# Optimization experiments

Hardware: AMD Instinct MI355X
Metric: run time of the kernel (lower is better)

## Reference

```python
import jax, jax.numpy as jnp
import numpy as np
from jax import lax


def setup_inputs() -> dict:
    key = jax.random.key(0)
    ks = jax.random.split(key, 8)
    B, S, H, L = 64, 512, 768, 9
    hidden = jax.random.normal(ks[0], (B, S, H), jnp.float32)
    label = jax.random.randint(ks[1], (B, S), 0, L, dtype=jnp.int32)
    mask = jnp.ones((B, S), jnp.int32)
    W = jax.random.normal(ks[2], (H, L), jnp.float32) * 0.02
    b = jnp.zeros((L,), jnp.float32)
    start_transitions = jax.random.normal(ks[3], (L,), jnp.float32) * 0.1
    end_transitions = jax.random.normal(ks[4], (L,), jnp.float32) * 0.1
    transitions = jax.random.normal(ks[5], (L, L), jnp.float32) * 0.1
    return dict(hidden=hidden, label=label, mask=mask, W=W, b=b,
                start_transitions=start_transitions,
                end_transitions=end_transitions,
                transitions=transitions)


def reference(hidden, label, mask, W, b, start_transitions, end_transitions, transitions):
    B, S, H = hidden.shape
    L = b.shape[0]
    # output_layer: [B,S,H] @ [H,L] -> emissions, then transpose to time-major [S,B,L]
    emissions = jnp.einsum('bsh,hl->bsl', hidden, W) + b
    em = jnp.transpose(emissions, (1, 0, 2))        # [S, B, L]
    tags = label.T                                   # [S, B]
    m = mask.T.astype(jnp.float32)                   # [S, B]

    def gather_tag(em_t, tag_t):
        # em_t [B,L], tag_t [B] -> [B]
        return jnp.take_along_axis(em_t, tag_t[:, None], axis=1)[:, 0]

    # ---- numerator: score of the gold path ----
    score0 = start_transitions[tags[0]] + gather_tag(em[0], tags[0])
    def num_step(carry, x):
        score, prev = carry
        em_t, tag_t, m_t = x
        s = transitions[prev, tag_t] + gather_tag(em_t, tag_t)
        score = score + s * m_t
        prev = jnp.where(m_t > 0, tag_t, prev)
        return (score, prev), None
    (score, last_gold), _ = lax.scan(num_step, (score0, tags[0]), (em[1:], tags[1:], m[1:]))
    score = score + end_transitions[last_gold]

    # ---- denominator: forward algorithm (logsumexp DP) ----
    alpha0 = start_transitions[None, :] + em[0]      # [B, L]
    def fwd_step(alpha, x):
        em_t, m_t = x
        nxt = jax.nn.logsumexp(alpha[:, :, None] + transitions[None, :, :] + em_t[:, None, :], axis=1)
        alpha = jnp.where(m_t[:, None] > 0, nxt, alpha)
        return alpha, None
    alphaT, _ = lax.scan(fwd_step, alpha0, (em[1:], m[1:]))
    logZ = jax.nn.logsumexp(alphaT + end_transitions[None, :], axis=1)

    llh = jnp.sum(score - logZ)                      # reduction='sum'
    loss = -llh / B

    # ---- Viterbi decode (decode() is called without mask -> full length) ----
    v0 = start_transitions[None, :] + em[0]
    def vit_step(v, em_t):
        scores = v[:, :, None] + transitions[None, :, :] + em_t[:, None, :]  # [B, L, L]
        return jnp.max(scores, axis=1), jnp.argmax(scores, axis=1)
    vT, hist = lax.scan(vit_step, v0, em[1:])        # hist [S-1, B, L]
    last_tag = jnp.argmax(vT + end_transitions[None, :], axis=1)  # [B]
    def back_step(tag, bp_t):
        prev = jnp.take_along_axis(bp_t, tag[:, None], axis=1)[:, 0]
        return prev, prev
    _, prevs = lax.scan(back_step, last_tag, hist, reverse=True)  # [S-1, B]
    path = jnp.concatenate([prevs, last_tag[None, :]], axis=0).T  # [B, S]

    # ---- accuracy bookkeeping (label > 0 mask) ----
    label_flat = label.reshape(-1)
    label_mask = (label_flat > 0).astype(jnp.int32)
    predict = path.reshape(-1).astype(jnp.int32) * label_mask
    correct = jnp.sum((predict == label_flat).astype(jnp.float32))
    return loss, correct, predict, label_flat
```

## Files before the change

kernel.cpp:

```cpp
#include <hip/hip_runtime.h>
#include <hip/hip_bf16.h>

#define NB 64
#define NS 512
#define NH 768
#define NL 9
#define NROWS (NB*NS)
#define EMN (NROWS*NL)

#define VST  4617
#define BPST 4616

__device__ __forceinline__ float readlane_f(float v, int l) {
    return __int_as_float(__builtin_amdgcn_readlane(__float_as_int(v), l));
}
__device__ __forceinline__ unsigned long long readlane_u64(unsigned long long v, int l) {
    unsigned int lo = (unsigned int)__builtin_amdgcn_readlane((int)(unsigned int)(v & 0xffffffffULL), l);
    unsigned int hi = (unsigned int)__builtin_amdgcn_readlane((int)(unsigned int)(v >> 32), l);
    return ((unsigned long long)hi << 32) | (unsigned long long)lo;
}
template <int CTRL>
__device__ __forceinline__ float dpp_add(float x) {
    int t = __builtin_amdgcn_update_dpp(0, __float_as_int(x), CTRL, 0xf, 0xf, false);
    return x + __int_as_float(t);
}
__device__ __forceinline__ float wave_sum_to63(float x) {
    x = dpp_add<0x111>(x);
    x = dpp_add<0x112>(x);
    x = dpp_add<0x114>(x);
    x = dpp_add<0x118>(x);
    x = dpp_add<0x142>(x);
    x = dpp_add<0x143>(x);
    return x;
}
template <int I>
__device__ __forceinline__ float rowbc(float x) {
    return __int_as_float(__builtin_amdgcn_ds_swizzle(__float_as_int(x), (I << 5) | 0x10));
}

__global__ __launch_bounds__(256) void k_gemm(const float* __restrict__ hidden,
                                              const float* __restrict__ W,
                                              const float* __restrict__ bias,
                                              float* __restrict__ em,
                                              float* __restrict__ out) {
    __shared__ float s_part[4][4][NL];
    int tid = threadIdx.x;
    int lane = tid & 63;
    int w = tid >> 6;
    int bx = blockIdx.x;
    if (bx == 0 && tid == 0) { out[0] = 0.f; out[1] = 0.f; }

    int kbase = 192 * w + lane;
    float Wv[3][NL];
#pragma unroll
    for (int c = 0; c < 3; c++) {
        const float* wp = W + (size_t)(kbase + 64 * c) * NL;
#pragma unroll
        for (int j = 0; j < NL; j++) Wv[c][j] = wp[j];
    }

#pragma unroll
    for (int r = 0; r < 4; r++) {
        int row = 4 * bx + r;
        const float* hp = hidden + (size_t)row * NH + kbase;
        float h0 = hp[0], h1 = hp[64], h2 = hp[128];
        float acc[NL];
#pragma unroll
        for (int j = 0; j < NL; j++) {
            acc[j] = fmaf(h0, Wv[0][j], fmaf(h1, Wv[1][j], h2 * Wv[2][j]));
        }
#pragma unroll
        for (int j = 0; j < NL; j++) acc[j] = wave_sum_to63(acc[j]);
        if (lane == 63) {
#pragma unroll
            for (int j = 0; j < NL; j++) s_part[w][r][j] = acc[j];
        }
    }
    __syncthreads();
    if (tid < 36) {
        int r = tid / NL, j = tid % NL;
        float v = (s_part[0][r][j] + s_part[1][r][j]) +
                  (s_part[2][r][j] + s_part[3][r][j]) + bias[j];
        em[(size_t)(4 * bx + r) * NL + j] = v;
    }
}

__global__ __launch_bounds__(256) void k_dp(const float* __restrict__ em,
                                            const int* __restrict__ label,
                                            const int* __restrict__ mask,
                                            const float* __restrict__ startT,
                                            const float* __restrict__ endT,
                                            const float* __restrict__ trans,
                                            float* __restrict__ out) {
    __shared__ float s_T[NL * NL];
    __shared__ int s_mki[4][NS];
    __shared__ float s_v[4 * VST];
    __shared__ unsigned char s_bp[4 * BPST];
    __shared__ unsigned char s_path[4 * NS];

    int bx = blockIdx.x;
    int tid = threadIdx.x;
    int lane = tid & 63;
    bool isfwd = bx < 16;
    int b0 = (isfwd ? bx : (bx - 16)) * 4;

    if (tid < NL * NL) s_T[tid] = trans[tid];
    if (isfwd) {
        for (int q = tid; q < 4 * NS / 4; q += 256)
            ((int4*)s_mki)[q] = ((const int4*)(mask + b0 * NS))[q];
    }
    __syncthreads();

    if (isfwd) {
        if (tid < 64) {
            int bb = lane >> 4;
            int jcol = lane & 15;
            int jcol9 = jcol < NL ? jcol : NL - 1;
            const float* gp = em + (size_t)(b0 + bb) * (NS * NL) + jcol9;
            float Mc0 = __expf(s_T[0 * NL + jcol9]);
            float Mc1 = __expf(s_T[1 * NL + jcol9]);
            float Mc2 = __expf(s_T[2 * NL + jcol9]);
            float Mc3 = __expf(s_T[3 * NL + jcol9]);
            float Mc4 = __expf(s_T[4 * NL + jcol9]);
            float Mc5 = __expf(s_T[5 * NL + jcol9]);
            float Mc6 = __expf(s_T[6 * NL + jcol9]);
            float Mc7 = __expf(s_T[7 * NL + jcol9]);
            float Mc8 = __expf(s_T[8 * NL + jcol9]);
            float a = __expf(startT[jcol9] + gp[0]);
            int eacc = 0;

#define FBODY(EC_, KC_) do { \
    float _w0=rowbc<0>(a),_w1=rowbc<1>(a),_w2=rowbc<2>(a),_w3=rowbc<3>(a),_w4=rowbc<4>(a), \
          _w5=rowbc<5>(a),_w6=rowbc<6>(a),_w7=rowbc<7>(a),_w8=rowbc<8>(a); \
    float _p0=_w0*Mc0,_p1=_w1*Mc1,_p2=_w2*Mc2,_p3=_w3*Mc3,_p4=_w4*Mc4, \
          _p5=_w5*Mc5,_p6=_w6*Mc6,_p7=_w7*Mc7,_p8=_w8*Mc8; \
    float _s=(((_p0+_p1)+(_p2+_p3))+((_p4+_p5)+(_p6+_p7)))+_p8; \
    float _an=(EC_)*_s; \
    a = ((KC_) > 0) ? _an : a; \
} while (0)

#define FREN() do { \
    float _c0=rowbc<0>(a),_c1=rowbc<1>(a),_c2=rowbc<2>(a),_c3=rowbc<3>(a),_c4=rowbc<4>(a), \
          _c5=rowbc<5>(a),_c6=rowbc<6>(a),_c7=rowbc<7>(a),_c8=rowbc<8>(a); \
    float _cc=(((_c0+_c1)+(_c2+_c3))+((_c4+_c5)+(_c6+_c7)))+_c8; \
    int _ex=((__float_as_int(_cc)>>23)&255)-127; \
    a=ldexpf(a,-_ex); eacc+=_ex; \
} while (0)

            float e8[8]; int k8[8];
#pragma unroll
            for (int p = 0; p < 8; p++) {
                e8[p] = __expf(gp[(1 + p) * NL]);
                k8[p] = s_mki[bb][1 + p];
            }
            for (int t0 = 1; t0 <= NS - 15; t0 += 8) {
#pragma unroll
                for (int p = 0; p < 8; p++) {
                    int t = t0 + p;
                    float ec = e8[p]; int kc = k8[p];
                    int tn = t + 8; tn = tn > NS - 1 ? NS - 1 : tn;
                    e8[p] = __expf(gp[tn * NL]);
                    k8[p] = s_mki[bb][tn];
                    FBODY(ec, kc);
                    if (p == 7) FREN();
                }
            }
#pragma unroll
            for (int p = 0; p < 7; p++) FBODY(e8[p], k8[p]);
#undef FBODY
#undef FREN
            float z = a * __expf(endT[jcol9]);
            float c0 = rowbc<0>(z), c1 = rowbc<1>(z), c2 = rowbc<2>(z);
            float c3 = rowbc<3>(z), c4 = rowbc<4>(z), c5 = rowbc<5>(z);
            float c6 = rowbc<6>(z), c7 = rowbc<7>(z), c8 = rowbc<8>(z);
            float c = (((c0 + c1) + (c2 + c3)) + ((c4 + c5) + (c6 + c7))) + c8;
            if (jcol == 0) {
                float lz = (float)eacc * 0.6931471805599453f + __logf(c);
                atomicAdd(out, lz * (1.0f / (float)NB));
            }
        } else if (tid < 128) {
            int g = lane >> 4;
            int ll = lane & 15;
            int b = b0 + g;
            const int* lb = label + b * NS;
            const float* ge = em + (size_t)b * NS * NL;
            int h = 0, sl = 0;
            for (int cch = 0; cch < 4; cch++) {
                int la8[8]; int mk8[8];
#pragma unroll
                for (int r = 0; r < 8; r++) {
                    int t = ll * 32 + cch * 8 + r;
                    la8[r] = lb[t];
                    int m = s_mki[g][t];
                    if (t == 0) m = 1;
                    mk8[r] = m;
                }
#pragma unroll
                for (int r = 0; r < 8; r++) if (mk8[r] > 0) { h = 1; sl = la8[r]; }
            }
#pragma unroll
            for (int d = 1; d < 16; d <<= 1) {
                int ho = __shfl_up(h, d, 16);
                int so = __shfl_up(sl, d, 16);
                if (!h) { h = ho; sl = so; }
            }
            int lg = __shfl(sl, 15, 16);
            int incoming = __shfl_up(sl, 1, 16);
            int labz = lb[0];
            int prevr = (ll == 0) ? labz : incoming;
            float sc = 0.f;
            for (int cch = 0; cch < 4; cch++) {
                int la8[8]; int mk8[8]; float ev8[8];
#pragma unroll
                for (int r = 0; r < 8; r++) {
                    int t = ll * 32 + cch * 8 + r;
                    la8[r] = lb[t];
                    int m = s_mki[g][t];
                    if (t == 0) m = 1;
                    mk8[r] = m;
                }
#pragma unroll
                for (int r = 0; r < 8; r++) {
                    int t = ll * 32 + cch * 8 + r;
                    ev8[r] = ge[t * NL + la8[r]];
                }
#pragma unroll
                for (int r = 0; r < 8; r++) {
                    int t = ll * 32 + cch * 8 + r;
                    if (t > 0) {
                        float s = s_T[prevr * NL + la8[r]] + ev8[r];
                        sc += s * (float)mk8[r];
                    }
                    if (mk8[r] > 0) prevr = la8[r];
                }
            }
            if (ll == 0) sc += startT[labz] + ge[labz] + endT[lg];
#pragma unroll
            for (int d = 1; d < 16; d <<= 1) sc += __shfl_xor(sc, d, 16);
            if (ll == 0) atomicAdd(out, -sc * (1.0f / (float)NB));
        }
    } else {
        if (tid < 64) {
            int bb = lane >> 4;
            int jcol = lane & 15;
            int jcol9 = jcol < NL ? jcol : NL - 1;
            const float* gv = em + (size_t)(b0 + bb) * (NS * NL) + jcol9;
            float Tc0 = s_T[0 * NL + jcol9];
            float Tc1 = s_T[1 * NL + jcol9];
            float Tc2 = s_T[2 * NL + jcol9];
            float Tc3 = s_T[3 * NL + jcol9];
            float Tc4 = s_T[4 * NL + jcol9];
            float Tc5 = s_T[5 * NL + jcol9];
            float Tc6 = s_T[6 * NL + jcol9];
            float Tc7 = s_T[7 * NL + jcol9];
            float Tc8 = s_T[8 * NL + jcol9];
            float v = startT[jcol9] + gv[0];
            int svbase = bb * VST + jcol;
            s_v[svbase] = v;

#define VBODY(EC_, T_) do { \
    float _w0=rowbc<0>(v),_w1=rowbc<1>(v),_w2=rowbc<2>(v),_w3=rowbc<3>(v),_w4=rowbc<4>(v), \
          _w5=rowbc<5>(v),_w6=rowbc<6>(v),_w7=rowbc<7>(v),_w8=rowbc<8>(v); \
    float _m0=_w0+Tc0,_m1=_w1+Tc1,_m2=_w2+Tc2,_m3=_w3+Tc3,_m4=_w4+Tc4, \
          _m5=_w5+Tc5,_m6=_w6+Tc6,_m7=_w7+Tc7,_m8=_w8+Tc8; \
    float _Ma=fmaxf(fmaxf(_m0,_m1),_m2); \
    float _Mb=fmaxf(fmaxf(_m3,_m4),_m5); \
    float _Mc=fmaxf(fmaxf(_m6,_m7),_m8); \
    v = fmaxf(fmaxf(_Ma,_Mb),_Mc) + (EC_); \
    s_v[svbase + (T_) * NL] = v; \
} while (0)

            float e8[8];
#pragma unroll
            for (int p = 0; p < 8; p++) e8[p] = gv[(1 + p) * NL];
            for (int t0 = 1; t0 <= NS - 15; t0 += 8) {
#pragma unroll
                for (int p = 0; p < 8; p++) {
                    int t = t0 + p;
                    float ec = e8[p];
                    int tn = t + 8; tn = tn > NS - 1 ? NS - 1 : tn;
                    e8[p] = gv[tn * NL];
                    VBODY(ec, t);
                }
            }
#pragma unroll
            for (int p = 0; p < 7; p++) VBODY(e8[p], 505 + p);
#undef VBODY
        }
        __syncthreads();
        for (int it = 0; it < 8; it++) {
            int item = tid + it * 256;
            int bb = item >> 9;
            int t = item & (NS - 1);
            if (t > 0) {
                const float* vpp = s_v + bb * VST + (t - 1) * NL;
                const float* ge = em + (size_t)(b0 + bb) * (NS * NL) + t * NL;
                float vp[NL], emt[NL];
#pragma unroll
                for (int i = 0; i < NL; i++) vp[i] = vpp[i];
#pragma unroll
                for (int j = 0; j < NL; j++) emt[j] = ge[j];
#pragma unroll
                for (int j = 0; j < NL; j++) {
                    float e = emt[j];
                    float val[NL];
#pragma unroll
                    for (int i = 0; i < NL; i++) val[i] = (vp[i] + s_T[i * NL + j]) + e;
                    bool c01 = val[0] >= val[1]; float m01 = c01 ? val[0] : val[1]; int i01 = c01 ? 0 : 1;
                    bool c23 = val[2] >= val[3]; float m23 = c23 ? val[2] : val[3]; int i23 = c23 ? 2 : 3;
                    bool c45 = val[4] >= val[5]; float m45 = c45 ? val[4] : val[5]; int i45 = c45 ? 4 : 5;
                    bool c67 = val[6] >= val[7]; float m67 = c67 ? val[6] : val[7]; int i67 = c67 ? 6 : 7;
                    bool ca = m01 >= m23; float ma = ca ? m01 : m23; int ia = ca ? i01 : i23;
                    bool cb = m45 >= m67; float mb = cb ? m45 : m67; int ib = cb ? i45 : i67;
                    bool cc = ma >= mb;  float mc = cc ? ma : mb;  int ic = cc ? ia : ib;
                    bool cd = mc >= val[8]; int bi = cd ? ic : 8;
                    s_bp[bb * BPST + t * NL + j] = (unsigned char)bi;
                }
            }
        }
        __syncthreads();
        {
            int w = tid >> 6;
            const float* sv = s_v + w * VST;
            const unsigned char* bpp = s_bp + w * BPST;
            unsigned char* pth = s_path + w * NS;
            float bb2 = sv[(NS - 1) * NL + 0] + endT[0]; int lt = 0;
#pragma unroll
            for (int jj = 1; jj < NL; jj++) {
                float fj = sv[(NS - 1) * NL + jj] + endT[jj];
                if (fj > bb2) { bb2 = fj; lt = jj; }
            }
            unsigned long long G[8];
#pragma unroll
            for (int r = 0; r < 8; r++) {
                int t0 = (lane * 8 + r) * NL;
                unsigned long long g = 0;
                if (lane == 0 && r == 0) {
                    g = 0x876543210ULL;
                } else {
#pragma unroll
                    for (int x = 0; x < NL; x++) g |= (unsigned long long)bpp[t0 + x] << (4 * x);
                }
                G[r] = g;
            }
            unsigned long long A = 0x876543210ULL;
#pragma unroll
            for (int r = 7; r >= 0; r--) {
                unsigned long long An = 0;
#pragma unroll
                for (int x = 0; x < NL; x++) {
                    int ax = (int)((A >> (4 * x)) & 15ULL);
                    int gvv = (int)((G[r] >> (4 * ax)) & 15ULL);
                    An |= (unsigned long long)gvv << (4 * x);
                }
                A = An;
            }
            int e = 0; int cur = lt;
            for (int llv = 63; llv >= 0; --llv) {
                if (lane == llv) e = cur;
                unsigned long long Al = readlane_u64(A, llv);
                cur = (int)((Al >> (4 * cur)) & 15ULL);
            }
            unsigned long long pw = 0; int c2 = e;
#pragma unroll
            for (int r = 7; r >= 0; r--) {
                pw |= (unsigned long long)c2 << (8 * r);
                c2 = (int)((G[r] >> (4 * c2)) & 15ULL);
            }
            *(unsigned long long*)(pth + lane * 8) = pw;
        }
        __syncthreads();
        float cnt = 0.f;
#pragma unroll
        for (int q = 0; q < 8; q++) {
            int item = tid + q * 256;
            int bb = item >> 9;
            int t = item & (NS - 1);
            int b = b0 + bb;
            int idx = b * NS + t;
            int lab = label[idx];
            int p = (int)s_path[bb * NS + t];
            int pred = (lab > 0) ? p : 0;
            out[2 + idx] = (float)pred;
            out[2 + NROWS + idx] = (float)lab;
            cnt += (pred == lab) ? 1.f : 0.f;
        }
#pragma unroll
        for (int d = 1; d < 64; d <<= 1) cnt += __shfl_xor(cnt, d);
        if ((tid & 63) == 0) atomicAdd(out + 1, cnt);
    }
}

extern "C" void kernel_launch(void* const* d_in, const int* in_sizes, int n_in,
                              void* d_out, int out_size, void* d_ws, size_t ws_size,
                              hipStream_t stream) {
    const float* hidden = (const float*)d_in[0];
    const int*   label  = (const int*)d_in[1];
    const int*   mask   = (const int*)d_in[2];
    const float* W      = (const float*)d_in[3];
    const float* bias   = (const float*)d_in[4];
    const float* startT = (const float*)d_in[5];
    const float* endT   = (const float*)d_in[6];
    const float* trans  = (const float*)d_in[7];
    float* out = (float*)d_out;

    float* em = (float*)d_ws;

    k_gemm<<<8192, 256, 0, stream>>>(hidden, W, bias, em, out);
    k_dp<<<32, 256, 0, stream>>>(em, label, mask, startT, endT, trans, out);
}
```

Measured before the change: 210.9 us.

## Interleave forward-algorithm and Viterbi recurrences in one wavefront per batch group

```diff
diff --git a/kernel.cpp b/kernel.cpp
--- a/kernel.cpp
+++ b/kernel.cpp
@@ -101,294 +101,259 @@
     int bx = blockIdx.x;
     int tid = threadIdx.x;
     int lane = tid & 63;
-    bool isfwd = bx < 16;
-    int b0 = (isfwd ? bx : (bx - 16)) * 4;
+    int b0 = bx * 4;
 
     if (tid < NL * NL) s_T[tid] = trans[tid];
-    if (isfwd) {
-        for (int q = tid; q < 4 * NS / 4; q += 256)
-            ((int4*)s_mki)[q] = ((const int4*)(mask + b0 * NS))[q];
-    }
-    __syncthreads();
-
-    if (isfwd) {
-        if (tid < 64) {
-            int bb = lane >> 4;
-            int jcol = lane & 15;
-            int jcol9 = jcol < NL ? jcol : NL - 1;
-            const float* gp = em + (size_t)(b0 + bb) * (NS * NL) + jcol9;
-            float Mc0 = __expf(s_T[0 * NL + jcol9]);
-            float Mc1 = __expf(s_T[1 * NL + jcol9]);
-            float Mc2 = __expf(s_T[2 * NL + jcol9]);
-            float Mc3 = __expf(s_T[3 * NL + jcol9]);
-            float Mc4 = __expf(s_T[4 * NL + jcol9]);
-            float Mc5 = __expf(s_T[5 * NL + jcol9]);
-            float Mc6 = __expf(s_T[6 * NL + jcol9]);
-            float Mc7 = __expf(s_T[7 * NL + jcol9]);
-            float Mc8 = __expf(s_T[8 * NL + jcol9]);
-            float a = __expf(startT[jcol9] + gp[0]);
-            int eacc = 0;
-
-#define FBODY(EC_, KC_) do { \
-    float _w0=rowbc<0>(a),_w1=rowbc<1>(a),_w2=rowbc<2>(a),_w3=rowbc<3>(a),_w4=rowbc<4>(a), \
-          _w5=rowbc<5>(a),_w6=rowbc<6>(a),_w7=rowbc<7>(a),_w8=rowbc<8>(a); \
-    float _p0=_w0*Mc0,_p1=_w1*Mc1,_p2=_w2*Mc2,_p3=_w3*Mc3,_p4=_w4*Mc4, \
-          _p5=_w5*Mc5,_p6=_w6*Mc6,_p7=_w7*Mc7,_p8=_w8*Mc8; \
-    float _s=(((_p0+_p1)+(_p2+_p3))+((_p4+_p5)+(_p6+_p7)))+_p8; \
-    float _an=(EC_)*_s; \
-    a = ((KC_) > 0) ? _an : a; \
-} while (0)
-
-#define FREN() do { \
-    float _c0=rowbc<0>(a),_c1=rowbc<1>(a),_c2=rowbc<2>(a),_c3=rowbc<3>(a),_c4=rowbc<4>(a), \
-          _c5=rowbc<5>(a),_c6=rowbc<6>(a),_c7=rowbc<7>(a),_c8=rowbc<8>(a); \
-    float _cc=(((_c0+_c1)+(_c2+_c3))+((_c4+_c5)+(_c6+_c7)))+_c8; \
-    int _ex=((__float_as_int(_cc)>>23)&255)-127; \
-    a=ldexpf(a,-_ex); eacc+=_ex; \
-} while (0)
-
-            float e8[8]; int k8[8];
-#pragma unroll
-            for (int p = 0; p < 8; p++) {
-                e8[p] = __expf(gp[(1 + p) * NL]);
-                k8[p] = s_mki[bb][1 + p];
-            }
-            for (int t0 = 1; t0 <= NS - 15; t0 += 8) {
-#pragma unroll
-                for (int p = 0; p < 8; p++) {
-                    int t = t0 + p;
-                    float ec = e8[p]; int kc = k8[p];
-                    int tn = t + 8; tn = tn > NS - 1 ? NS - 1 : tn;
-                    e8[p] = __expf(gp[tn * NL]);
-                    k8[p] = s_mki[bb][tn];
-                    FBODY(ec, kc);
-                    if (p == 7) FREN();
-                }
-            }
-#pragma unroll
-            for (int p = 0; p < 7; p++) FBODY(e8[p], k8[p]);
-#undef FBODY
-#undef FREN
-            float z = a * __expf(endT[jcol9]);
-            float c0 = rowbc<0>(z), c1 = rowbc<1>(z), c2 = rowbc<2>(z);
-            float c3 = rowbc<3>(z), c4 = rowbc<4>(z), c5 = rowbc<5>(z);
-            float c6 = rowbc<6>(z), c7 = rowbc<7>(z), c8 = rowbc<8>(z);
-            float c = (((c0 + c1) + (c2 + c3)) + ((c4 + c5) + (c6 + c7))) + c8;
-            if (jcol == 0) {
-                float lz = (float)eacc * 0.6931471805599453f + __logf(c);
-                atomicAdd(out, lz * (1.0f / (float)NB));
-            }
-        } else if (tid < 128) {
-            int g = lane >> 4;
-            int ll = lane & 15;
-            int b = b0 + g;
-            const int* lb = label + b * NS;
-            const float* ge = em + (size_t)b * NS * NL;
-            int h = 0, sl = 0;
-            for (int cch = 0; cch < 4; cch++) {
-                int la8[8]; int mk8[8];
-#pragma unroll
-                for (int r = 0; r < 8; r++) {
-                    int t = ll * 32 + cch * 8 + r;
-                    la8[r] = lb[t];
-                    int m = s_mki[g][t];
-                    if (t == 0) m = 1;
-                    mk8[r] = m;
-                }
-#pragma unroll
-                for (int r = 0; r < 8; r++) if (mk8[r] > 0) { h = 1; sl = la8[r]; }
-            }
-#pragma unroll
-            for (int d = 1; d < 16; d <<= 1) {
-                int ho = __shfl_up(h, d, 16);
-                int so = __shfl_up(sl, d, 16);
-                if (!h) { h = ho; sl = so; }
-            }
-            int lg = __shfl(sl, 15, 16);
-            int incoming = __shfl_up(sl, 1, 16);
-            int labz = lb[0];
-            int prevr = (ll == 0) ? labz : incoming;
-            float sc = 0.f;
-            for (int cch = 0; cch < 4; cch++) {
-                int la8[8]; int mk8[8]; float ev8[8];
-#pragma unroll
-                for (int r = 0; r < 8; r++) {
-                    int t = ll * 32 + cch * 8 + r;
-                    la8[r] = lb[t];
-                    int m = s_mki[g][t];
-                    if (t == 0) m = 1;
-                    mk8[r] = m;
-                }
-#pragma unroll
-                for (int r = 0; r < 8; r++) {
-                    int t = ll * 32 + cch * 8 + r;
-                    ev8[r] = ge[t * NL + la8[r]];
-                }
-#pragma unroll
-                for (int r = 0; r < 8; r++) {
-                    int t = ll * 32 + cch * 8 + r;
-                    if (t > 0) {
-                        float s = s_T[prevr * NL + la8[r]] + ev8[r];
-                        sc += s * (float)mk8[r];
-                    }
-                    if (mk8[r] > 0) prevr = la8[r];
-                }
-            }
-            if (ll == 0) sc += startT[labz] + ge[labz] + endT[lg];
-#pragma unroll
-            for (int d = 1; d < 16; d <<= 1) sc += __shfl_xor(sc, d, 16);
-            if (ll == 0) atomicAdd(out, -sc * (1.0f / (float)NB));
-        }
-    } else {
-        if (tid < 64) {
-            int bb = lane >> 4;
-            int jcol = lane & 15;
-            int jcol9 = jcol < NL ? jcol : NL - 1;
-            const float* gv = em + (size_t)(b0 + bb) * (NS * NL) + jcol9;
-            float Tc0 = s_T[0 * NL + jcol9];
-            float Tc1 = s_T[1 * NL + jcol9];
-            float Tc2 = s_T[2 * NL + jcol9];
-            float Tc3 = s_T[3 * NL + jcol9];
-            float Tc4 = s_T[4 * NL + jcol9];
-            float Tc5 = s_T[5 * NL + jcol9];
-            float Tc6 = s_T[6 * NL + jcol9];
-            float Tc7 = s_T[7 * NL + jcol9];
-            float Tc8 = s_T[8 * NL + jcol9];
-            float v = startT[jcol9] + gv[0];
-            int svbase = bb * VST + jcol;
-            s_v[svbase] = v;
-
-#define VBODY(EC_, T_) do { \
-    float _w0=rowbc<0>(v),_w1=rowbc<1>(v),_w2=rowbc<2>(v),_w3=rowbc<3>(v),_w4=rowbc<4>(v), \
-          _w5=rowbc<5>(v),_w6=rowbc<6>(v),_w7=rowbc<7>(v),_w8=rowbc<8>(v); \
+    for (int q = tid; q < 4 * NS / 4; q += 256)
+        ((int4*)s_mki)[q] = ((const int4*)(mask + b0 * NS))[q];
+    __syncthreads();
+
+    if (tid < 64) {
+        int bb = lane >> 4;
+        int jcol = lane & 15;
+        int jcol9 = jcol < NL ? jcol : NL - 1;
+        const float* gp = em + (size_t)(b0 + bb) * (NS * NL) + jcol9;
+        float Mc0 = __expf(s_T[0 * NL + jcol9]), Tc0 = s_T[0 * NL + jcol9];
+        float Mc1 = __expf(s_T[1 * NL + jcol9]), Tc1 = s_T[1 * NL + jcol9];
+        float Mc2 = __expf(s_T[2 * NL + jcol9]), Tc2 = s_T[2 * NL + jcol9];
+        float Mc3 = __expf(s_T[3 * NL + jcol9]), Tc3 = s_T[3 * NL + jcol9];
+        float Mc4 = __expf(s_T[4 * NL + jcol9]), Tc4 = s_T[4 * NL + jcol9];
+        float Mc5 = __expf(s_T[5 * NL + jcol9]), Tc5 = s_T[5 * NL + jcol9];
+        float Mc6 = __expf(s_T[6 * NL + jcol9]), Tc6 = s_T[6 * NL + jcol9];
+        float Mc7 = __expf(s_T[7 * NL + jcol9]), Tc7 = s_T[7 * NL + jcol9];
+        float Mc8 = __expf(s_T[8 * NL + jcol9]), Tc8 = s_T[8 * NL + jcol9];
+        float st0 = startT[jcol9] + gp[0];
+        float a = __expf(st0);
+        float v = st0;
+        int eacc = 0;
+        int svbase = bb * VST + jcol;
+        s_v[svbase] = v;
+
+#define SWZ9(SRC_, A0,A1,A2,A3,A4,A5,A6,A7,A8) \
+    float A0 = rowbc<0>(SRC_), A1 = rowbc<1>(SRC_), A2 = rowbc<2>(SRC_); \
+    float A3 = rowbc<3>(SRC_), A4 = rowbc<4>(SRC_), A5 = rowbc<5>(SRC_); \
+    float A6 = rowbc<6>(SRC_), A7 = rowbc<7>(SRC_), A8 = rowbc<8>(SRC_)
+
+#define STEP(EV_, EF_, KC_, T_) do { \
+    SWZ9(v, _w0,_w1,_w2,_w3,_w4,_w5,_w6,_w7,_w8); \
+    SWZ9(a, _q0,_q1,_q2,_q3,_q4,_q5,_q6,_q7,_q8); \
     float _m0=_w0+Tc0,_m1=_w1+Tc1,_m2=_w2+Tc2,_m3=_w3+Tc3,_m4=_w4+Tc4, \
           _m5=_w5+Tc5,_m6=_w6+Tc6,_m7=_w7+Tc7,_m8=_w8+Tc8; \
     float _Ma=fmaxf(fmaxf(_m0,_m1),_m2); \
     float _Mb=fmaxf(fmaxf(_m3,_m4),_m5); \
     float _Mc=fmaxf(fmaxf(_m6,_m7),_m8); \
-    v = fmaxf(fmaxf(_Ma,_Mb),_Mc) + (EC_); \
+    v = fmaxf(fmaxf(_Ma,_Mb),_Mc) + (EV_); \
     s_v[svbase + (T_) * NL] = v; \
+    float _p0=_q0*Mc0,_p1=_q1*Mc1,_p2=_q2*Mc2,_p3=_q3*Mc3,_p4=_q4*Mc4, \
+          _p5=_q5*Mc5,_p6=_q6*Mc6,_p7=_q7*Mc7,_p8=_q8*Mc8; \
+    float _s=(((_p0+_p1)+(_p2+_p3))+((_p4+_p5)+(_p6+_p7)))+_p8; \
+    float _an=(EF_)*_s; \
+    a = ((KC_) > 0) ? _an : a; \
 } while (0)
 
-            float e8[8];
-#pragma unroll
-            for (int p = 0; p < 8; p++) e8[p] = gv[(1 + p) * NL];
-            for (int t0 = 1; t0 <= NS - 15; t0 += 8) {
-#pragma unroll
-                for (int p = 0; p < 8; p++) {
-                    int t = t0 + p;
-                    float ec = e8[p];
-                    int tn = t + 8; tn = tn > NS - 1 ? NS - 1 : tn;
-                    e8[p] = gv[tn * NL];
-                    VBODY(ec, t);
+#define FREN() do { \
+    SWZ9(a, _c0,_c1,_c2,_c3,_c4,_c5,_c6,_c7,_c8); \
+    float _cc=(((_c0+_c1)+(_c2+_c3))+((_c4+_c5)+(_c6+_c7)))+_c8; \
+    int _ex=((__float_as_int(_cc)>>23)&255)-127; \
+    a=ldexpf(a,-_ex); eacc+=_ex; \
+} while (0)
+
+        float ef8[8]; float ev8[8]; int k8[8];
+#pragma unroll
+        for (int p = 0; p < 8; p++) {
+            float raw = gp[(1 + p) * NL];
+            ev8[p] = raw;
+            ef8[p] = __expf(raw);
+            k8[p] = s_mki[bb][1 + p];
+        }
+        for (int t0 = 1; t0 <= NS - 15; t0 += 8) {
+#pragma unroll
+            for (int p = 0; p < 8; p++) {
+                int t = t0 + p;
+                float ecv = ev8[p]; float ecf = ef8[p]; int kc = k8[p];
+                int tn = t + 8; tn = tn > NS - 1 ? NS - 1 : tn;
+                float raw = gp[tn * NL];
+                ev8[p] = raw;
+                ef8[p] = __expf(raw);
+                k8[p] = s_mki[bb][tn];
+                STEP(ecv, ecf, kc, t);
+                if (p == 7) FREN();
+            }
+        }
+#pragma unroll
+        for (int p = 0; p < 7; p++) STEP(ev8[p], ef8[p], k8[p], 505 + p);
+#undef STEP
+#undef FREN
+        float z = a * __expf(endT[jcol9]);
+        SWZ9(z, zc0,zc1,zc2,zc3,zc4,zc5,zc6,zc7,zc8);
+        float c = (((zc0 + zc1) + (zc2 + zc3)) + ((zc4 + zc5) + (zc6 + zc7))) + zc8;
+        if (jcol == 0) {
+            float lz = (float)eacc * 0.6931471805599453f + __logf(c);
+            atomicAdd(out, lz * (1.0f / (float)NB));
+        }
+#undef SWZ9
+    } else if (tid < 128) {
+        int g = lane >> 4;
+        int ll = lane & 15;
+        int b = b0 + g;
+        const int* lb = label + b * NS;
+        const float* ge = em + (size_t)b * NS * NL;
+        int h = 0, sl = 0;
+        for (int cch = 0; cch < 4; cch++) {
+            int la8[8]; int mk8[8];
+#pragma unroll
+            for (int r = 0; r < 8; r++) {
+                int t = ll * 32 + cch * 8 + r;
+                la8[r] = lb[t];
+                int m = s_mki[g][t];
+                if (t == 0) m = 1;
+                mk8[r] = m;
+            }
+#pragma unroll
+            for (int r = 0; r < 8; r++) if (mk8[r] > 0) { h = 1; sl = la8[r]; }
+        }
+#pragma unroll
+        for (int d = 1; d < 16; d <<= 1) {
+            int ho = __shfl_up(h, d, 16);
+            int so = __shfl_up(sl, d, 16);
+            if (!h) { h = ho; sl = so; }
+        }
+        int lg = __shfl(sl, 15, 16);
+        int incoming = __shfl_up(sl, 1, 16);
+        int labz = lb[0];
+        int prevr = (ll == 0) ? labz : incoming;
+        float sc = 0.f;
+        for (int cch = 0; cch < 4; cch++) {
+            int la8[8]; int mk8[8]; float ev8[8];
+#pragma unroll
+            for (int r = 0; r < 8; r++) {
+                int t = ll * 32 + cch * 8 + r;
+                la8[r] = lb[t];
+                int m = s_mki[g][t];
+                if (t == 0) m = 1;
+                mk8[r] = m;
+            }
+#pragma unroll
+            for (int r = 0; r < 8; r++) {
+                int t = ll * 32 + cch * 8 + r;
+                ev8[r] = ge[t * NL + la8[r]];
+            }
+#pragma unroll
+            for (int r = 0; r < 8; r++) {
+                int t = ll * 32 + cch * 8 + r;
+                if (t > 0) {
+                    float s = s_T[prevr * NL + la8[r]] + ev8[r];
+                    sc += s * (float)mk8[r];
                 }
-            }
-#pragma unroll
-            for (int p = 0; p < 7; p++) VBODY(e8[p], 505 + p);
-#undef VBODY
-        }
-        __syncthreads();
-        for (int it = 0; it < 8; it++) {
-            int item = tid + it * 256;
-            int bb = item >> 9;
-            int t = item & (NS - 1);
-            if (t > 0) {
-                const float* vpp = s_v + bb * VST + (t - 1) * NL;
-                const float* ge = em + (size_t)(b0 + bb) * (NS * NL) + t * NL;
-                float vp[NL], emt[NL];
-#pragma unroll
-                for (int i = 0; i < NL; i++) vp[i] = vpp[i];
-#pragma unroll
-                for (int j = 0; j < NL; j++) emt[j] = ge[j];
-#pragma unroll
-                for (int j = 0; j < NL; j++) {
-                    float e = emt[j];
-                    float val[NL];
-#pragma unroll
-                    for (int i = 0; i < NL; i++) val[i] = (vp[i] + s_T[i * NL + j]) + e;
-                    bool c01 = val[0] >= val[1]; float m01 = c01 ? val[0] : val[1]; int i01 = c01 ? 0 : 1;
-                    bool c23 = val[2] >= val[3]; float m23 = c23 ? val[2] : val[3]; int i23 = c23 ? 2 : 3;
-                    bool c45 = val[4] >= val[5]; float m45 = c45 ? val[4] : val[5]; int i45 = c45 ? 4 : 5;
-                    bool c67 = val[6] >= val[7]; float m67 = c67 ? val[6] : val[7]; int i67 = c67 ? 6 : 7;
-                    bool ca = m01 >= m23; float ma = ca ? m01 : m23; int ia = ca ? i01 : i23;
-                    bool cb = m45 >= m67; float mb = cb ? m45 : m67; int ib = cb ? i45 : i67;
-                    bool cc = ma >= mb;  float mc = cc ? ma : mb;  int ic = cc ? ia : ib;
-                    bool cd = mc >= val[8]; int bi = cd ? ic : 8;
-                    s_bp[bb * BPST + t * NL + j] = (unsigned char)bi;
-                }
-            }
-        }
-        __syncthreads();
-        {
-            int w = tid >> 6;
-            const float* sv = s_v + w * VST;
-            const unsigned char* bpp = s_bp + w * BPST;
-            unsigned char* pth = s_path + w * NS;
-            float bb2 = sv[(NS - 1) * NL + 0] + endT[0]; int lt = 0;
-#pragma unroll
-            for (int jj = 1; jj < NL; jj++) {
-                float fj = sv[(NS - 1) * NL + jj] + endT[jj];
-                if (fj > bb2) { bb2 = fj; lt = jj; }
-            }
-            unsigned long long G[8];
-#pragma unroll
-            for (int r = 0; r < 8; r++) {
-                int t0 = (lane * 8 + r) * NL;
-                unsigned long long g = 0;
-                if (lane == 0 && r == 0) {
-                    g = 0x876543210ULL;
-                } else {
-#pragma unroll
-                    for (int x = 0; x < NL; x++) g |= (unsigned long long)bpp[t0 + x] << (4 * x);
-                }
-                G[r] = g;
-            }
-            unsigned long long A = 0x876543210ULL;
-#pragma unroll
-            for (int r = 7; r >= 0; r--) {
-                unsigned long long An = 0;
-#pragma unroll
-                for (int x = 0; x < NL; x++) {
-                    int ax = (int)((A >> (4 * x)) & 15ULL);
-                    int gvv = (int)((G[r] >> (4 * ax)) & 15ULL);
-                    An |= (unsigned long long)gvv << (4 * x);
-                }
-                A = An;
-            }
-            int e = 0; int cur = lt;
-            for (int llv = 63; llv >= 0; --llv) {
-                if (lane == llv) e = cur;
-                unsigned long long Al = readlane_u64(A, llv);
-                cur = (int)((Al >> (4 * cur)) & 15ULL);
-            }
-            unsigned long long pw = 0; int c2 = e;
-#pragma unroll
-            for (int r = 7; r >= 0; r--) {
-                pw |= (unsigned long long)c2 << (8 * r);
-                c2 = (int)((G[r] >> (4 * c2)) & 15ULL);
-            }
-            *(unsigned long long*)(pth + lane * 8) = pw;
-        }
-        __syncthreads();
-        float cnt = 0.f;
-#pragma unroll
-        for (int q = 0; q < 8; q++) {
-            int item = tid + q * 256;
-            int bb = item >> 9;
-            int t = item & (NS - 1);
-            int b = b0 + bb;
-            int idx = b * NS + t;
-            int lab = label[idx];
-            int p = (int)s_path[bb * NS + t];
-            int pred = (lab > 0) ? p : 0;
-            out[2 + idx] = (float)pred;
-            out[2 + NROWS + idx] = (float)lab;
-            cnt += (pred == lab) ? 1.f : 0.f;
-        }
-#pragma unroll
-        for (int d = 1; d < 64; d <<= 1) cnt += __shfl_xor(cnt, d);
-        if ((tid & 63) == 0) atomicAdd(out + 1, cnt);
-    }
+                if (mk8[r] > 0) prevr = la8[r];
+            }
+        }
+        if (ll == 0) sc += startT[labz] + ge[labz] + endT[lg];
+#pragma unroll
+        for (int d = 1; d < 16; d <<= 1) sc += __shfl_xor(sc, d, 16);
+        if (ll == 0) atomicAdd(out, -sc * (1.0f / (float)NB));
+    }
+    __syncthreads();
+    for (int it = 0; it < 8; it++) {
+        int item = tid + it * 256;
+        int bb = item >> 9;
+        int t = item & (NS - 1);
+        if (t > 0) {
+            const float* vpp = s_v + bb * VST + (t - 1) * NL;
+            const float* ge = em + (size_t)(b0 + bb) * (NS * NL) + t * NL;
+            float vp[NL], emt[NL];
+#pragma unroll
+            for (int i = 0; i < NL; i++) vp[i] = vpp[i];
+#pragma unroll
+            for (int j = 0; j < NL; j++) emt[j] = ge[j];
+#pragma unroll
+            for (int j = 0; j < NL; j++) {
+                float e = emt[j];
+                float val[NL];
+#pragma unroll
+                for (int i = 0; i < NL; i++) val[i] = (vp[i] + s_T[i * NL + j]) + e;
+                bool c01 = val[0] >= val[1]; float m01 = c01 ? val[0] : val[1]; int i01 = c01 ? 0 : 1;
+                bool c23 = val[2] >= val[3]; float m23 = c23 ? val[2] : val[3]; int i23 = c23 ? 2 : 3;
+                bool c45 = val[4] >= val[5]; float m45 = c45 ? val[4] : val[5]; int i45 = c45 ? 4 : 5;
+                bool c67 = val[6] >= val[7]; float m67 = c67 ? val[6] : val[7]; int i67 = c67 ? 6 : 7;
+                bool ca = m01 >= m23; float ma = ca ? m01 : m23; int ia = ca ? i01 : i23;
+                bool cb = m45 >= m67; float mb = cb ? m45 : m67; int ib = cb ? i45 : i67;
+                bool cc = ma >= mb;  float mc = cc ? ma : mb;  int ic = cc ? ia : ib;
+                bool cd = mc >= val[8]; int bi = cd ? ic : 8;
+                s_bp[bb * BPST + t * NL + j] = (unsigned char)bi;
+            }
+        }
+    }
+    __syncthreads();
+    {
+        int w = tid >> 6;
+        const float* sv = s_v + w * VST;
+        const unsigned char* bpp = s_bp + w * BPST;
+        unsigned char* pth = s_path + w * NS;
+        float bb2 = sv[(NS - 1) * NL + 0] + endT[0]; int lt = 0;
+#pragma unroll
+        for (int jj = 1; jj < NL; jj++) {
+            float fj = sv[(NS - 1) * NL + jj] + endT[jj];
+            if (fj > bb2) { bb2 = fj; lt = jj; }
+        }
+        unsigned long long G[8];
+#pragma unroll
+        for (int r = 0; r < 8; r++) {
+            int t0 = (lane * 8 + r) * NL;
+            unsigned long long g = 0;
+            if (lane == 0 && r == 0) {
+                g = 0x876543210ULL;
+            } else {
+#pragma unroll
+                for (int x = 0; x < NL; x++) g |= (unsigned long long)bpp[t0 + x] << (4 * x);
+            }
+            G[r] = g;
+        }
+        unsigned long long A = 0x876543210ULL;
+#pragma unroll
+        for (int r = 7; r >= 0; r--) {
+            unsigned long long An = 0;
+#pragma unroll
+            for (int x = 0; x < NL; x++) {
+                int ax = (int)((A >> (4 * x)) & 15ULL);
+                int gvv = (int)((G[r] >> (4 * ax)) & 15ULL);
+                An |= (unsigned long long)gvv << (4 * x);
+            }
+            A = An;
+        }
+        int e = 0; int cur = lt;
+        for (int llv = 63; llv >= 0; --llv) {
+            if (lane == llv) e = cur;
+            unsigned long long Al = readlane_u64(A, llv);
+            cur = (int)((Al >> (4 * cur)) & 15ULL);
+        }
+        unsigned long long pw = 0; int c2 = e;
+#pragma unroll
+        for (int r = 7; r >= 0; r--) {
+            pw |= (unsigned long long)c2 << (8 * r);
+            c2 = (int)((G[r] >> (4 * c2)) & 15ULL);
+        }
+        *(unsigned long long*)(pth + lane * 8) = pw;
+    }
+    __syncthreads();
+    float cnt = 0.f;
+#pragma unroll
+    for (int q = 0; q < 8; q++) {
+        int item = tid + q * 256;
+        int bb = item >> 9;
+        int t = item & (NS - 1);
+        int b = b0 + bb;
+        int idx = b * NS + t;
+        int lab = label[idx];
+        int p = (int)s_path[bb * NS + t];
+        int pred = (lab > 0) ? p : 0;
+        out[2 + idx] = (float)pred;
+        out[2 + NROWS + idx] = (float)lab;
+        cnt += (pred == lab) ? 1.f : 0.f;
+    }
+#pragma unroll
+    for (int d = 1; d < 64; d <<= 1) cnt += __shfl_xor(cnt, d);
+    if ((tid & 63) == 0) atomicAdd(out + 1, cnt);
 }
 
 extern "C" void kernel_launch(void* const* d_in, const int* in_sizes, int n_in,
@@ -407,5 +372,5 @@
     float* em = (float*)d_ws;
 
     k_gemm<<<8192, 256, 0, stream>>>(hidden, W, bias, em, out);
-    k_dp<<<32, 256, 0, stream>>>(em, label, mask, startT, endT, trans, out);
-}
+    k_dp<<<16, 256, 0, stream>>>(em, label, mask, startT, endT, trans, out);
+}
```

Measured after the change: 246.8 us. +17.0%, slower.

## Fuse emission GEMM and CRF DP into one kernel with per-chunk readiness flags

Applied to the files above, without the earlier changes.

```diff
diff --git a/kernel.cpp b/kernel.cpp
--- a/kernel.cpp
+++ b/kernel.cpp
@@ -7,6 +7,7 @@
 #define NL 9
 #define NROWS (NB*NS)
 #define EMN (NROWS*NL)
+#define NGEMM 8192
 
 #define VST  4617
 #define BPST 4616
@@ -36,6 +37,385 @@
 template <int I>
 __device__ __forceinline__ float rowbc(float x) {
     return __int_as_float(__builtin_amdgcn_ds_swizzle(__float_as_int(x), (I << 5) | 0x10));
+}
+__device__ __forceinline__ void poll8(unsigned int* fp) {
+    int guard = 0;
+    while (atomicAdd(fp, 0u) < 8u) {
+        __builtin_amdgcn_s_sleep(32);
+        if (++guard > (1 << 20)) break;
+    }
+}
+
+__global__ __launch_bounds__(256) void k_fused(const float* __restrict__ hidden,
+                                               const float* __restrict__ W,
+                                               const float* __restrict__ bias,
+                                               float* __restrict__ em,
+                                               unsigned int* __restrict__ flags,
+                                               float* __restrict__ vglob,
+                                               const int* __restrict__ label,
+                                               const int* __restrict__ mask,
+                                               const float* __restrict__ startT,
+                                               const float* __restrict__ endT,
+                                               const float* __restrict__ trans,
+                                               float* __restrict__ out) {
+    __shared__ float s_part[4][4][NL];
+    __shared__ float s_T[NL * NL];
+    __shared__ int s_mki[4][NS];
+    __shared__ unsigned char s_bp[4 * BPST];
+    __shared__ unsigned char s_path[4 * NS];
+
+    int bx = blockIdx.x;
+    int tid = threadIdx.x;
+    int lane = tid & 63;
+
+    if (bx < NGEMM) {
+        int w = tid >> 6;
+        int tq = bx >> 6;
+        int b  = bx & 63;
+        int kbase = 192 * w + lane;
+        float Wv[3][NL];
+#pragma unroll
+        for (int c = 0; c < 3; c++) {
+            const float* wp = W + (size_t)(kbase + 64 * c) * NL;
+#pragma unroll
+            for (int j = 0; j < NL; j++) Wv[c][j] = wp[j];
+        }
+#pragma unroll
+        for (int r = 0; r < 4; r++) {
+            int row = b * NS + 4 * tq + r;
+            const float* hp = hidden + (size_t)row * NH + kbase;
+            float h0 = hp[0], h1 = hp[64], h2 = hp[128];
+            float acc[NL];
+#pragma unroll
+            for (int j = 0; j < NL; j++) {
+                acc[j] = fmaf(h0, Wv[0][j], fmaf(h1, Wv[1][j], h2 * Wv[2][j]));
+            }
+#pragma unroll
+            for (int j = 0; j < NL; j++) acc[j] = wave_sum_to63(acc[j]);
+            if (lane == 63) {
+#pragma unroll
+                for (int j = 0; j < NL; j++) s_part[w][r][j] = acc[j];
+            }
+        }
+        __syncthreads();
+        if (tid < 36) {
+            int r = tid / NL, j = tid % NL;
+            float v = (s_part[0][r][j] + s_part[1][r][j]) +
+                      (s_part[2][r][j] + s_part[3][r][j]) + bias[j];
+            em[(size_t)(b * NS + 4 * tq + r) * NL + j] = v;
+        }
+        if (tid == 0) {
+            __threadfence();
+            atomicAdd(&flags[b * 16 + (tq >> 3)], 1u);
+        }
+        return;
+    }
+
+    int dpb = bx - NGEMM;
+    bool isfwd = dpb < 16;
+    int b0 = (isfwd ? dpb : (dpb - 16)) * 4;
+
+    if (tid < NL * NL) s_T[tid] = trans[tid];
+    if (isfwd) {
+        for (int q = tid; q < 4 * NS / 4; q += 256)
+            ((int4*)s_mki)[q] = ((const int4*)(mask + b0 * NS))[q];
+    }
+    __syncthreads();
+
+    if (isfwd) {
+        if (tid < 64) {
+            int bb = lane >> 4;
+            int jcol = lane & 15;
+            int jcol9 = jcol < NL ? jcol : NL - 1;
+            unsigned int* fbase = flags + (size_t)(b0 + bb) * 16;
+            poll8(fbase + 0);
+            __threadfence();
+            const float* gp = em + (size_t)(b0 + bb) * (NS * NL) + jcol9;
+            float Mc0 = __expf(s_T[0 * NL + jcol9]);
+            float Mc1 = __expf(s_T[1 * NL + jcol9]);
+            float Mc2 = __expf(s_T[2 * NL + jcol9]);
+            float Mc3 = __expf(s_T[3 * NL + jcol9]);
+            float Mc4 = __expf(s_T[4 * NL + jcol9]);
+            float Mc5 = __expf(s_T[5 * NL + jcol9]);
+            float Mc6 = __expf(s_T[6 * NL + jcol9]);
+            float Mc7 = __expf(s_T[7 * NL + jcol9]);
+            float Mc8 = __expf(s_T[8 * NL + jcol9]);
+            float a = __expf(startT[jcol9] + gp[0]);
+            int eacc = 0;
+
+#define FBODY(EC_, KC_) do { \
+    float _w0=rowbc<0>(a),_w1=rowbc<1>(a),_w2=rowbc<2>(a),_w3=rowbc<3>(a),_w4=rowbc<4>(a), \
+          _w5=rowbc<5>(a),_w6=rowbc<6>(a),_w7=rowbc<7>(a),_w8=rowbc<8>(a); \
+    float _p0=_w0*Mc0,_p1=_w1*Mc1,_p2=_w2*Mc2,_p3=_w3*Mc3,_p4=_w4*Mc4, \
+          _p5=_w5*Mc5,_p6=_w6*Mc6,_p7=_w7*Mc7,_p8=_w8*Mc8; \
+    float _s=(((_p0+_p1)+(_p2+_p3))+((_p4+_p5)+(_p6+_p7)))+_p8; \
+    float _an=(EC_)*_s; \
+    a = ((KC_) > 0) ? _an : a; \
+} while (0)
+
+#define FREN() do { \
+    float _c0=rowbc<0>(a),_c1=rowbc<1>(a),_c2=rowbc<2>(a),_c3=rowbc<3>(a),_c4=rowbc<4>(a), \
+          _c5=rowbc<5>(a),_c6=rowbc<6>(a),_c7=rowbc<7>(a),_c8=rowbc<8>(a); \
+    float _cc=(((_c0+_c1)+(_c2+_c3))+((_c4+_c5)+(_c6+_c7)))+_c8; \
+    int _ex=((__float_as_int(_cc)>>23)&255)-127; \
+    a=ldexpf(a,-_ex); eacc+=_ex; \
+} while (0)
+
+            float e8[8]; int k8[8];
+#pragma unroll
+            for (int p = 0; p < 8; p++) {
+                e8[p] = __expf(gp[(1 + p) * NL]);
+                k8[p] = s_mki[bb][1 + p];
+            }
+            int ready = 0;
+            for (int t0 = 1; t0 <= NS - 15; t0 += 8) {
+                int cneed = (t0 + 15) >> 5; cneed = cneed > 15 ? 15 : cneed;
+                if (cneed != ready) { poll8(fbase + cneed); __threadfence(); ready = cneed; }
+#pragma unroll
+                for (int p = 0; p < 8; p++) {
+                    int t = t0 + p;
+                    float ec = e8[p]; int kc = k8[p];
+                    int tn = t + 8; tn = tn > NS - 1 ? NS - 1 : tn;
+                    e8[p] = __expf(gp[tn * NL]);
+                    k8[p] = s_mki[bb][tn];
+                    FBODY(ec, kc);
+                    if (p == 7) FREN();
+                }
+            }
+#pragma unroll
+            for (int p = 0; p < 7; p++) FBODY(e8[p], k8[p]);
+#undef FBODY
+#undef FREN
+            float z = a * __expf(endT[jcol9]);
+            float c0 = rowbc<0>(z), c1 = rowbc<1>(z), c2 = rowbc<2>(z);
+            float c3 = rowbc<3>(z), c4 = rowbc<4>(z), c5 = rowbc<5>(z);
+            float c6 = rowbc<6>(z), c7 = rowbc<7>(z), c8 = rowbc<8>(z);
+            float c = (((c0 + c1) + (c2 + c3)) + ((c4 + c5) + (c6 + c7))) + c8;
+            if (jcol == 0) {
+                float lz = (float)eacc * 0.6931471805599453f + __logf(c);
+                atomicAdd(out, lz * (1.0f / (float)NB));
+            }
+        } else if (tid < 128) {
+            int g = lane >> 4;
+            int ll = lane & 15;
+            int b = b0 + g;
+            unsigned int* fbase = flags + (size_t)b * 16;
+            for (int c = 0; c < 16; c++) poll8(fbase + c);
+            __threadfence();
+            const int* lb = label + b * NS;
+            const float* ge = em + (size_t)b * NS * NL;
+            int h = 0, sl = 0;
+            for (int cch = 0; cch < 4; cch++) {
+                int la8[8]; int mk8[8];
+#pragma unroll
+                for (int r = 0; r < 8; r++) {
+                    int t = ll * 32 + cch * 8 + r;
+                    la8[r] = lb[t];
+                    int m = s_mki[g][t];
+                    if (t == 0) m = 1;
+                    mk8[r] = m;
+                }
+#pragma unroll
+                for (int r = 0; r < 8; r++) if (mk8[r] > 0) { h = 1; sl = la8[r]; }
+            }
+#pragma unroll
+            for (int d = 1; d < 16; d <<= 1) {
+                int ho = __shfl_up(h, d, 16);
+                int so = __shfl_up(sl, d, 16);
+                if (!h) { h = ho; sl = so; }
+            }
+            int lg = __shfl(sl, 15, 16);
+            int incoming = __shfl_up(sl, 1, 16);
+            int labz = lb[0];
+            int prevr = (ll == 0) ? labz : incoming;
+            float sc = 0.f;
+            for (int cch = 0; cch < 4; cch++) {
+                int la8[8]; int mk8[8]; float ev8[8];
+#pragma unroll
+                for (int r = 0; r < 8; r++) {
+                    int t = ll * 32 + cch * 8 + r;
+                    la8[r] = lb[t];
+                    int m = s_mki[g][t];
+                    if (t == 0) m = 1;
+                    mk8[r] = m;
+                }
+#pragma unroll
+                for (int r = 0; r < 8; r++) {
+                    int t = ll * 32 + cch * 8 + r;
+                    ev8[r] = ge[t * NL + la8[r]];
+                }
+#pragma unroll
+                for (int r = 0; r < 8; r++) {
+                    int t = ll * 32 + cch * 8 + r;
+                    if (t > 0) {
+                        float s = s_T[prevr * NL + la8[r]] + ev8[r];
+                        sc += s * (float)mk8[r];
+                    }
+                    if (mk8[r] > 0) prevr = la8[r];
+                }
+            }
+            if (ll == 0) sc += startT[labz] + ge[labz] + endT[lg];
+#pragma unroll
+            for (int d = 1; d < 16; d <<= 1) sc += __shfl_xor(sc, d, 16);
+            if (ll == 0) atomicAdd(out, -sc * (1.0f / (float)NB));
+        }
+    } else {
+        if (tid < 64) {
+            int bb = lane >> 4;
+            int jcol = lane & 15;
+            int jcol9 = jcol < NL ? jcol : NL - 1;
+            unsigned int* fbase = flags + (size_t)(b0 + bb) * 16;
+            poll8(fbase + 0);
+            __threadfence();
+            const float* gv = em + (size_t)(b0 + bb) * (NS * NL) + jcol9;
+            float* vg = vglob + (size_t)(b0 + bb) * VST;
+            float Tc0 = s_T[0 * NL + jcol9];
+            float Tc1 = s_T[1 * NL + jcol9];
+            float Tc2 = s_T[2 * NL + jcol9];
+            float Tc3 = s_T[3 * NL + jcol9];
+            float Tc4 = s_T[4 * NL + jcol9];
+            float Tc5 = s_T[5 * NL + jcol9];
+            float Tc6 = s_T[6 * NL + jcol9];
+            float Tc7 = s_T[7 * NL + jcol9];
+            float Tc8 = s_T[8 * NL + jcol9];
+            float v = startT[jcol9] + gv[0];
+            if (jcol < NL) vg[jcol] = v;
+
+#define VBODY(EC_, T_) do { \
+    float _w0=rowbc<0>(v),_w1=rowbc<1>(v),_w2=rowbc<2>(v),_w3=rowbc<3>(v),_w4=rowbc<4>(v), \
+          _w5=rowbc<5>(v),_w6=rowbc<6>(v),_w7=rowbc<7>(v),_w8=rowbc<8>(v); \
+    float _m0=_w0+Tc0,_m1=_w1+Tc1,_m2=_w2+Tc2,_m3=_w3+Tc3,_m4=_w4+Tc4, \
+          _m5=_w5+Tc5,_m6=_w6+Tc6,_m7=_w7+Tc7,_m8=_w8+Tc8; \
+    float _Ma=fmaxf(fmaxf(_m0,_m1),_m2); \
+    float _Mb=fmaxf(fmaxf(_m3,_m4),_m5); \
+    float _Mc=fmaxf(fmaxf(_m6,_m7),_m8); \
+    v = fmaxf(fmaxf(_Ma,_Mb),_Mc) + (EC_); \
+    if (jcol < NL) vg[(T_) * NL + jcol] = v; \
+} while (0)
+
+            float e8[8];
+#pragma unroll
+            for (int p = 0; p < 8; p++) e8[p] = gv[(1 + p) * NL];
+            int ready = 0;
+            for (int t0 = 1; t0 <= NS - 15; t0 += 8) {
+                int cneed = (t0 + 15) >> 5; cneed = cneed > 15 ? 15 : cneed;
+                if (cneed != ready) { poll8(fbase + cneed); __threadfence(); ready = cneed; }
+#pragma unroll
+                for (int p = 0; p < 8; p++) {
+                    int t = t0 + p;
+                    float ec = e8[p];
+                    int tn = t + 8; tn = tn > NS - 1 ? NS - 1 : tn;
+                    e8[p] = gv[tn * NL];
+                    VBODY(ec, t);
+                }
+            }
+#pragma unroll
+            for (int p = 0; p < 7; p++) VBODY(e8[p], 505 + p);
+#undef VBODY
+        }
+        __syncthreads();
+        __threadfence();
+        for (int it = 0; it < 8; it++) {
+            int item = tid + it * 256;
+            int bb = item >> 9;
+            int t = item & (NS - 1);
+            if (t > 0) {
+                const float* vpp = vglob + (size_t)(b0 + bb) * VST + (t - 1) * NL;
+                const float* ge = em + (size_t)(b0 + bb) * (NS * NL) + t * NL;
+                float vp[NL], emt[NL];
+#pragma unroll
+                for (int i = 0; i < NL; i++) vp[i] = vpp[i];
+#pragma unroll
+                for (int j = 0; j < NL; j++) emt[j] = ge[j];
+#pragma unroll
+                for (int j = 0; j < NL; j++) {
+                    float e = emt[j];
+                    float val[NL];
+#pragma unroll
+                    for (int i = 0; i < NL; i++) val[i] = (vp[i] + s_T[i * NL + j]) + e;
+                    bool c01 = val[0] >= val[1]; float m01 = c01 ? val[0] : val[1]; int i01 = c01 ? 0 : 1;
+                    bool c23 = val[2] >= val[3]; float m23 = c23 ? val[2] : val[3]; int i23 = c23 ? 2 : 3;
+                    bool c45 = val[4] >= val[5]; float m45 = c45 ? val[4] : val[5]; int i45 = c45 ? 4 : 5;
+                    bool c67 = val[6] >= val[7]; float m67 = c67 ? val[6] : val[7]; int i67 = c67 ? 6 : 7;
+                    bool ca = m01 >= m23; float ma = ca ? m01 : m23; int ia = ca ? i01 : i23;
+                    bool cb = m45 >= m67; float mb = cb ? m45 : m67; int ib = cb ? i45 : i67;
+                    bool cc = ma >= mb;  float mc = cc ? ma : mb;  int ic = cc ? ia : ib;
+                    bool cd = mc >= val[8]; int bi = cd ? ic : 8;
+                    s_bp[bb * BPST + t * NL + j] = (unsigned char)bi;
+                }
+            }
+        }
+        __syncthreads();
+        {
+            int w = tid >> 6;
+            const float* sv = vglob + (size_t)(b0 + w) * VST;
+            const unsigned char* bpp = s_bp + w * BPST;
+            unsigned char* pth = s_path + w * NS;
+            float bb2 = sv[(NS - 1) * NL + 0] + endT[0]; int lt = 0;
+#pragma unroll
+            for (int jj = 1; jj < NL; jj++) {
+                float fj = sv[(NS - 1) * NL + jj] + endT[jj];
+                if (fj > bb2) { bb2 = fj; lt = jj; }
+            }
+            unsigned long long G[8];
+#pragma unroll
+            for (int r = 0; r < 8; r++) {
+                int t0 = (lane * 8 + r) * NL;
+                unsigned long long g = 0;
+                if (lane == 0 && r == 0) {
+                    g = 0x876543210ULL;
+                } else {
+#pragma unroll
+                    for (int x = 0; x < NL; x++) g |= (unsigned long long)bpp[t0 + x] << (4 * x);
+                }
+                G[r] = g;
+            }
+            unsigned long long A = 0x876543210ULL;
+#pragma unroll
+            for (int r = 7; r >= 0; r--) {
+                unsigned long long An = 0;
+#pragma unroll
+                for (int x = 0; x < NL; x++) {
+                    int ax = (int)((A >> (4 * x)) & 15ULL);
+                    int gvv = (int)((G[r] >> (4 * ax)) & 15ULL);
+                    An |= (unsigned long long)gvv << (4 * x);
+                }
+                A = An;
+            }
+            int e = 0; int cur = lt;
+            for (int llv = 63; llv >= 0; --llv) {
+                if (lane == llv) e = cur;
+                unsigned long long Al = readlane_u64(A, llv);
+                cur = (int)((Al >> (4 * cur)) & 15ULL);
+            }
+            unsigned long long pw = 0; int c2 = e;
+#pragma unroll
+            for (int r = 7; r >= 0; r--) {
+                pw |= (unsigned long long)c2 << (8 * r);
+                c2 = (int)((G[r] >> (4 * c2)) & 15ULL);
+            }
+            *(unsigned long long*)(pth + lane * 8) = pw;
+        }
+        __syncthreads();
+        float cnt = 0.f;
+#pragma unroll
+        for (int q = 0; q < 8; q++) {
+            int item = tid + q * 256;
+            int bb = item >> 9;
+            int t = item & (NS - 1);
+            int b = b0 + bb;
+            int idx = b * NS + t;
+            int lab = label[idx];
+            int p = (int)s_path[bb * NS + t];
+            int pred = (lab > 0) ? p : 0;
+            out[2 + idx] = (float)pred;
+            out[2 + NROWS + idx] = (float)lab;
+            cnt += (pred == lab) ? 1.f : 0.f;
+        }
+#pragma unroll
+        for (int d = 1; d < 64; d <<= 1) cnt += __shfl_xor(cnt, d);
+        if ((tid & 63) == 0) atomicAdd(out + 1, cnt);
+    }
 }
 
 __global__ __launch_bounds__(256) void k_gemm(const float* __restrict__ hidden,
@@ -49,7 +429,6 @@
     int w = tid >> 6;
     int bx = blockIdx.x;
     if (bx == 0 && tid == 0) { out[0] = 0.f; out[1] = 0.f; }
-
     int kbase = 192 * w + lane;
     float Wv[3][NL];
 #pragma unroll
@@ -58,7 +437,6 @@
 #pragma unroll
         for (int j = 0; j < NL; j++) Wv[c][j] = wp[j];
     }
-
 #pragma unroll
     for (int r = 0; r < 4; r++) {
         int row = 4 * bx + r;
@@ -128,7 +506,6 @@
             float Mc8 = __expf(s_T[8 * NL + jcol9]);
             float a = __expf(startT[jcol9] + gp[0]);
             int eacc = 0;
-
 #define FBODY(EC_, KC_) do { \
     float _w0=rowbc<0>(a),_w1=rowbc<1>(a),_w2=rowbc<2>(a),_w3=rowbc<3>(a),_w4=rowbc<4>(a), \
           _w5=rowbc<5>(a),_w6=rowbc<6>(a),_w7=rowbc<7>(a),_w8=rowbc<8>(a); \
@@ -138,7 +515,6 @@
     float _an=(EC_)*_s; \
     a = ((KC_) > 0) ? _an : a; \
 } while (0)
-
 #define FREN() do { \
     float _c0=rowbc<0>(a),_c1=rowbc<1>(a),_c2=rowbc<2>(a),_c3=rowbc<3>(a),_c4=rowbc<4>(a), \
           _c5=rowbc<5>(a),_c6=rowbc<6>(a),_c7=rowbc<7>(a),_c8=rowbc<8>(a); \
@@ -146,7 +522,6 @@
     int _ex=((__float_as_int(_cc)>>23)&255)-127; \
     a=ldexpf(a,-_ex); eacc+=_ex; \
 } while (0)
-
             float e8[8]; int k8[8];
 #pragma unroll
             for (int p = 0; p < 8; p++) {
@@ -257,7 +632,6 @@
             float v = startT[jcol9] + gv[0];
             int svbase = bb * VST + jcol;
             s_v[svbase] = v;
-
 #define VBODY(EC_, T_) do { \
     float _w0=rowbc<0>(v),_w1=rowbc<1>(v),_w2=rowbc<2>(v),_w3=rowbc<3>(v),_w4=rowbc<4>(v), \
           _w5=rowbc<5>(v),_w6=rowbc<6>(v),_w7=rowbc<7>(v),_w8=rowbc<8>(v); \
@@ -269,7 +643,6 @@
     v = fmaxf(fmaxf(_Ma,_Mb),_Mc) + (EC_); \
     s_v[svbase + (T_) * NL] = v; \
 } while (0)
-
             float e8[8];
 #pragma unroll
             for (int p = 0; p < 8; p++) e8[p] = gv[(1 + p) * NL];
@@ -405,7 +778,17 @@
     float* out = (float*)d_out;
 
     float* em = (float*)d_ws;
-
-    k_gemm<<<8192, 256, 0, stream>>>(hidden, W, bias, em, out);
-    k_dp<<<32, 256, 0, stream>>>(em, label, mask, startT, endT, trans, out);
-}
+    unsigned int* flags = (unsigned int*)(em + EMN);
+    float* vglob = (float*)((char*)flags + 4096);
+    size_t need = (size_t)EMN * 4 + 4096 + (size_t)64 * VST * 4;
+
+    if (ws_size >= need) {
+        hipMemsetAsync(flags, 0, 4096, stream);
+        hipMemsetAsync(d_out, 0, 8, stream);
+        k_fused<<<NGEMM + 32, 256, 0, stream>>>(hidden, W, bias, em, flags, vglob,
+                                                label, mask, startT, endT, trans, out);
+    } else {
+        k_gemm<<<8192, 256, 0, stream>>>(hidden, W, bias, em, out);
+        k_dp<<<32, 256, 0, stream>>>(em, label, mask, startT, endT, trans, out);
+    }
+}
```

Result: slower. 561.5 us (+166.2%).
